# Performance work log

Hardware: AMD Instinct MI355X
Metric: run time of the kernel (lower is better)

## Reference

```python
import jax, jax.numpy as jnp
import numpy as np

B, T = 1024, 1024
D_IN, UNITS, WIDTH, DEPTH, D_OUT = 6, 64, 128, 3, 6
START = UNITS + D_IN  # concat([x_normed, h]) width
EPS = 1e-8


def _xavier(key, fin, fout):
    lim = float(np.sqrt(6.0 / (fin + fout)))
    return jax.random.uniform(key, (fin, fout), minval=-lim, maxval=lim, dtype=jnp.float32)


def setup_inputs() -> dict:
    key = jax.random.key(0)
    ks = jax.random.split(key, 12)
    d = {
        "x": jax.random.normal(ks[0], (B, T, D_IN), dtype=jnp.float32),
        "init_F": jax.random.normal(ks[1], (B, 2 + UNITS), dtype=jnp.float32) * 0.1,
    }
    dims = [START] + [WIDTH] * DEPTH
    for i in range(DEPTH):
        d[f"qb1_w{i}"] = _xavier(ks[2 + 2 * i], dims[i], dims[i + 1])
        d[f"qb1_b{i}"] = jnp.zeros((dims[i + 1],), dtype=jnp.float32)
        d[f"qb2_w{i}"] = _xavier(ks[3 + 2 * i], dims[i], dims[i + 1])
        d[f"qb2_b{i}"] = jnp.zeros((dims[i + 1],), dtype=jnp.float32)
    d["wa"] = _xavier(ks[8], WIDTH, UNITS)
    d["ba"] = jnp.zeros((UNITS,), dtype=jnp.float32)
    d["wb"] = _xavier(ks[9], WIDTH, UNITS)
    d["bb"] = jnp.zeros((UNITS,), dtype=jnp.float32)
    # fc_out bias is frozen at zero in the original -> weight only
    d["wout"] = _xavier(ks[10], UNITS, D_OUT)
    return d


def reference(x, init_F,
              qb1_w0, qb1_b0, qb2_w0, qb2_b0,
              qb1_w1, qb1_b1, qb2_w1, qb2_b1,
              qb1_w2, qb1_b2, qb2_w2, qb2_b2,
              wa, ba, wb, bb, wout):
    layers = ((qb1_w0, qb1_b0, qb2_w0, qb2_b0),
              (qb1_w1, qb1_b1, qb2_w1, qb2_b1),
              (qb1_w2, qb1_b2, qb2_w2, qb2_b2))
    h0 = init_F[:, 2:2 + UNITS]  # [B, UNITS]

    def step(h, xt):  # xt: [B, D_IN], h: [B, UNITS]
        norm = jnp.sqrt(jnp.sum(xt * xt, axis=1, keepdims=True))  # [B,1]
        xn = xt / (norm + EPS)
        c = jnp.concatenate([xn, h], axis=1)  # [B, START]
        for i, (w1, b1, w2, b2) in enumerate(layers):
            x1 = c @ w1 + b1
            x2 = c @ w2 + b2
            if i < DEPTH - 1:
                x1 = jnp.tanh(x1)
                x2 = jnp.tanh(x2)
            c = x1 * x2
        g = jnp.tanh(c)
        alpha = jnp.exp(g @ wa + ba)          # [B, UNITS]
        beta = jnp.tanh(g @ wb + bb)          # [B, UNITS]
        h_new = jnp.exp(-alpha * norm) * (h - beta) + beta
        return h_new, (h_new @ wout, alpha)

    _, (outs, alphas) = jax.lax.scan(step, h0, jnp.swapaxes(x, 0, 1))
    # outs: [T,B,D_OUT], alphas: [T,B,UNITS] -> batch-major
    return jnp.swapaxes(outs, 0, 1), jnp.swapaxes(alphas, 0, 1)
```

## Files before the change

kernel.cpp:

```cpp
#include <hip/hip_runtime.h>
#include <stdint.h>
#include <stddef.h>

#define NB 1024
#define TB 1024
#define D_IN 6
#define UNITS 64
#define WIDTH 128
#define DOUT 6
#define EPSF 1e-8f
#define SPB 16
#define LDK0 108
#define LDK 140

typedef _Float16 v8h __attribute__((ext_vector_type(8)));
typedef float v4f __attribute__((ext_vector_type(4)));

#define MFMAH(A,Bf,C) __builtin_amdgcn_mfma_f32_16x16x32_f16((A),(Bf),(C),0,0,0)

#define BARRIER_LDS() asm volatile("s_waitcnt lgkmcnt(0)\n\ts_barrier" ::: "memory")

#define C2L2E  2.8853900817779268f
#define L2E    1.4426950408889634f
#define NEGL2E (-1.4426950408889634f)

__device__ __forceinline__ float rcp_fast(float x){ return __builtin_amdgcn_rcpf(x); }

__device__ __forceinline__ float tanh_from_arg(float a2){
  float u = __builtin_amdgcn_exp2f(a2);
  return fmaf(-2.0f, rcp_fast(u + 1.0f), 1.0f);
}

__device__ __forceinline__ void make_frag1(const float* vals, v8h& hv){
  #pragma unroll
  for (int j = 0; j < 8; j++) hv[j] = (_Float16)vals[j];
}
__device__ __forceinline__ void make_frag2(const float* vals, v8h& hv, v8h& lv){
  #pragma unroll
  for (int j = 0; j < 8; j++){
    _Float16 h = (_Float16)vals[j];
    hv[j] = h;
    lv[j] = (_Float16)(vals[j] - (float)h);
  }
}

__global__ __launch_bounds__(512, 2) void lmsc_kernel(
    const float* __restrict__ x, const float* __restrict__ initF,
    const float* __restrict__ w10, const float* __restrict__ b10,
    const float* __restrict__ w20, const float* __restrict__ b20,
    const float* __restrict__ w11, const float* __restrict__ b11,
    const float* __restrict__ w21, const float* __restrict__ b21,
    const float* __restrict__ w12, const float* __restrict__ b12,
    const float* __restrict__ w22, const float* __restrict__ b22,
    const float* __restrict__ wa, const float* __restrict__ ba,
    const float* __restrict__ wb, const float* __restrict__ bb,
    const float* __restrict__ wo,
    float* __restrict__ outs, float* __restrict__ alph)
{
  __shared__ __attribute__((aligned(16))) _Float16 c0[2][SPB*LDK0];
  __shared__ __attribute__((aligned(16))) _Float16 cP[SPB*LDK];
  __shared__ __attribute__((aligned(16))) _Float16 cQ[SPB*LDK];
  __shared__ __attribute__((aligned(16))) _Float16 cG[SPB*LDK];
  __shared__ __attribute__((aligned(16))) float nrm[2][SPB];

  const int tid = threadIdx.x;
  const int wv = tid >> 6;
  const int ln = tid & 63;
  const int mn = ln & 15;
  const int qd = ln >> 4;
  const int q8 = qd * 8;
  const int n  = wv * 16 + mn;
  const int sgbase = (int)blockIdx.x * SPB;

  float tmp[8];


  v8h B0[3][2];
  #pragma unroll
  for (int kf = 0; kf < 3; kf++)
    #pragma unroll
    for (int br = 0; br < 2; br++){
      const float* W = br ? w20 : w10;
      #pragma unroll
      for (int j = 0; j < 8; j++){
        int k = kf*32 + q8 + j;
        int r = (k < 6) ? k : ((k >= 8 && k < 72) ? (k - 2) : -1);
        tmp[j] = (r >= 0) ? W[r*WIDTH + n] * C2L2E : 0.0f;
      }
      make_frag1(tmp, B0[kf][br]);
    }

  v8h B1[4][2], B2[4][2];
  #pragma unroll
  for (int kf = 0; kf < 4; kf++)
    #pragma unroll
    for (int br = 0; br < 2; br++){
      const float* W = br ? w21 : w11;
      #pragma unroll
      for (int j = 0; j < 8; j++)
        tmp[j] = W[(kf*32 + q8 + j)*WIDTH + n] * C2L2E;
      make_frag1(tmp, B1[kf][br]);
      const float* V = br ? w22 : w12;
      const float sc = br ? 1.0f : C2L2E;
      #pragma unroll
      for (int j = 0; j < 8; j++)
        tmp[j] = V[(kf*32 + q8 + j)*WIDTH + n] * sc;
      make_frag1(tmp, B2[kf][br]);
    }

  const int u = (wv & 3) * 16 + mn;
  v8h Bah[4], Bal[4], Bbh[4];
  #pragma unroll
  for (int kf = 0; kf < 4; kf++){
    #pragma unroll
    for (int j = 0; j < 8; j++)
      tmp[j] = wa[(kf*32 + q8 + j)*UNITS + u] * L2E;
    make_frag2(tmp, Bah[kf], Bal[kf]);
    #pragma unroll
    for (int j = 0; j < 8; j++)
      tmp[j] = wb[(kf*32 + q8 + j)*UNITS + u] * C2L2E;
    make_frag1(tmp, Bbh[kf]);
  }
  const float bsa = ba[u] * L2E;
  const float bsb = bb[u] * C2L2E;

  v8h Woh0, Woh1;
  #pragma unroll
  for (int j = 0; j < 8; j++)
    tmp[j] = (mn < DOUT) ? wo[(q8 + j)*DOUT + mn] : 0.0f;
  make_frag1(tmp, Woh0);
  #pragma unroll
  for (int j = 0; j < 8; j++)
    tmp[j] = (mn < DOUT) ? wo[(32 + q8 + j)*DOUT + mn] : 0.0f;
  make_frag1(tmp, Woh1);

  const float e0a = b10[n] * C2L2E, e0b = b20[n] * C2L2E;
  const float e1a = b11[n] * C2L2E, e1b = b21[n] * C2L2E;
  const float e2a = b12[n] * C2L2E, e2b = b22[n];

  float* alp  = alph + ((size_t)(sgbase + qd*4) * TB) * UNITS + u;
  float* outp = outs + ((size_t)(sgbase + qd*4) * TB) * DOUT + mn;

  for (int i = tid; i < 2*SPB*LDK0; i += 512) c0[0][i] = (_Float16)0.0f;
  __syncthreads();

  float hreg[4];
  if (wv < 4){
    #pragma unroll
    for (int r = 0; r < 4; r++){
      int s = qd*4 + r;
      float v = initF[(size_t)(sgbase + s)*(2 + UNITS) + 2 + u];
      hreg[r] = v;
      c0[0][s*LDK0 + 8 + u] = (_Float16)v;
    }
  }
  float xv0=0, xv1=0, xv2=0, xv3=0, xv4=0, xv5=0;
  if (wv == 4 && ln < 16){
    const float* xp = x + (size_t)(sgbase + ln)*TB*D_IN;
    float a0=xp[0], a1=xp[1], a2=xp[2], a3=xp[3], a4=xp[4], a5=xp[5];
    float nv = sqrtf(a0*a0 + a1*a1 + a2*a2 + a3*a3 + a4*a4 + a5*a5);
    nrm[0][ln] = nv * NEGL2E;
    float inv = 1.0f / (nv + EPSF);
    c0[0][ln*LDK0 + 0] = (_Float16)(a0*inv);
    c0[0][ln*LDK0 + 1] = (_Float16)(a1*inv);
    c0[0][ln*LDK0 + 2] = (_Float16)(a2*inv);
    c0[0][ln*LDK0 + 3] = (_Float16)(a3*inv);
    c0[0][ln*LDK0 + 4] = (_Float16)(a4*inv);
    c0[0][ln*LDK0 + 5] = (_Float16)(a5*inv);
    xv0 = xp[6]; xv1 = xp[7]; xv2 = xp[8]; xv3 = xp[9]; xv4 = xp[10]; xv5 = xp[11];
  }
  __syncthreads();

  auto wout_phase = [&](const _Float16* cb, int tt){
    v8h ah0 = *(const v8h*)(cb + mn*LDK0 + 8 + q8);
    v8h ah1 = *(const v8h*)(cb + mn*LDK0 + 40 + q8);
    v4f acc = {0.f, 0.f, 0.f, 0.f};
    acc = MFMAH(ah0, Woh0, acc);
    acc = MFMAH(ah1, Woh1, acc);
    if (mn < DOUT){
      #pragma unroll
      for (int r = 0; r < 4; r++)
        outp[(size_t)r*TB*DOUT + (size_t)tt*DOUT] = acc[r];
    }
  };

  for (int t = 0; t < TB; t++){
    const int p = t & 1;
    const _Float16* c0r = c0[p];
    _Float16* c0w = c0[p ^ 1];

    {
      v8h ah[3];
      #pragma unroll
      for (int kf = 0; kf < 3; kf++)
        ah[kf] = *(const v8h*)(c0r + mn*LDK0 + kf*32 + q8);
      v4f acc0 = {e0a, e0a, e0a, e0a};
      v4f acc1 = {e0b, e0b, e0b, e0b};
      #pragma unroll
      for (int kf = 0; kf < 3; kf++){
        acc0 = MFMAH(ah[kf], B0[kf][0], acc0);
        acc1 = MFMAH(ah[kf], B0[kf][1], acc1);
      }
      #pragma unroll
      for (int r = 0; r < 4; r++){
        float u0 = __builtin_amdgcn_exp2f(acc0[r]);
        float u1 = __builtin_amdgcn_exp2f(acc1[r]);
        float pr = u0 * u1;
        float sm = u0 + u1;
        float pp = pr + 1.0f;
        float res = (pp - sm) * rcp_fast(pp + sm);
        cP[(qd*4 + r)*LDK + n] = (_Float16)res;
      }
    }
    BARRIER_LDS();

    {
      v8h ah[4];
      #pragma unroll
      for (int kf = 0; kf < 4; kf++)
        ah[kf] = *(const v8h*)(cP + mn*LDK + kf*32 + q8);
      v4f acc0 = {e1a, e1a, e1a, e1a};
      v4f acc1 = {e1b, e1b, e1b, e1b};
      #pragma unroll
      for (int kf = 0; kf < 4; kf++){
        acc0 = MFMAH(ah[kf], B1[kf][0], acc0);
        acc1 = MFMAH(ah[kf], B1[kf][1], acc1);
      }
      #pragma unroll
      for (int r = 0; r < 4; r++){
        float u0 = __builtin_amdgcn_exp2f(acc0[r]);
        float u1 = __builtin_amdgcn_exp2f(acc1[r]);
        float pr = u0 * u1;
        float sm = u0 + u1;
        float pp = pr + 1.0f;
        float res = (pp - sm) * rcp_fast(pp + sm);
        cQ[(qd*4 + r)*LDK + n] = (_Float16)res;
      }
    }
    BARRIER_LDS();

    {
      v8h ah[4];
      #pragma unroll
      for (int kf = 0; kf < 4; kf++)
        ah[kf] = *(const v8h*)(cQ + mn*LDK + kf*32 + q8);
      v4f acc0 = {e2a, e2a, e2a, e2a};
      v4f acc1 = {e2b, e2b, e2b, e2b};
      #pragma unroll
      for (int kf = 0; kf < 4; kf++){
        acc0 = MFMAH(ah[kf], B2[kf][0], acc0);
        acc1 = MFMAH(ah[kf], B2[kf][1], acc1);
      }
      #pragma unroll
      for (int r = 0; r < 4; r++)
        cG[(qd*4 + r)*LDK + n] = (_Float16)tanh_from_arg(acc0[r] * acc1[r]);
    }
    BARRIER_LDS();

    if (wv < 4){
      v8h gh[4];
      #pragma unroll
      for (int kf = 0; kf < 4; kf++)
        gh[kf] = *(const v8h*)(cG + mn*LDK + kf*32 + q8);
      v4f pA0 = {bsa, bsa, bsa, bsa};
      v4f pA1 = {0.f, 0.f, 0.f, 0.f};
      v4f pB  = {bsb, bsb, bsb, bsb};
      #pragma unroll
      for (int kf = 0; kf < 2; kf++){
        pA0 = MFMAH(gh[kf], Bah[kf], pA0);
        pA0 = MFMAH(gh[kf], Bal[kf], pA0);
        pA1 = MFMAH(gh[kf+2], Bah[kf+2], pA1);
        pA1 = MFMAH(gh[kf+2], Bal[kf+2], pA1);
        pB  = MFMAH(gh[2*kf],   Bbh[2*kf],   pB);
        pB  = MFMAH(gh[2*kf+1], Bbh[2*kf+1], pB);
      }
      #pragma unroll
      for (int r = 0; r < 4; r++){
        int s = qd*4 + r;
        float m = nrm[p][s];
        float alpha = __builtin_amdgcn_exp2f(pA0[r] + pA1[r]);
        float beta  = tanh_from_arg(pB[r]);
        float dec   = __builtin_amdgcn_exp2f(alpha * m);
        float h = fmaf(dec, hreg[r] - beta, beta);
        hreg[r] = h;
        c0w[s*LDK0 + 8 + u] = (_Float16)h;
        alp[(size_t)r*TB*UNITS] = alpha;
      }
      alp += UNITS;
    } else if (wv == 7){
      if (t > 0) wout_phase(c0r, t - 1);
    } else if (wv == 4 && ln < 16){
      float nv2 = sqrtf(xv0*xv0 + xv1*xv1 + xv2*xv2 + xv3*xv3 + xv4*xv4 + xv5*xv5);
      nrm[p ^ 1][ln] = nv2 * NEGL2E;
      float inv = 1.0f / (nv2 + EPSF);
      c0w[ln*LDK0 + 0] = (_Float16)(xv0*inv);
      c0w[ln*LDK0 + 1] = (_Float16)(xv1*inv);
      c0w[ln*LDK0 + 2] = (_Float16)(xv2*inv);
      c0w[ln*LDK0 + 3] = (_Float16)(xv3*inv);
      c0w[ln*LDK0 + 4] = (_Float16)(xv4*inv);
      c0w[ln*LDK0 + 5] = (_Float16)(xv5*inv);
      int tn = t + 2; if (tn > TB - 1) tn = TB - 1;
      const float* xp = x + ((size_t)(sgbase + ln)*TB + (size_t)tn)*D_IN;
      xv0 = xp[0]; xv1 = xp[1]; xv2 = xp[2]; xv3 = xp[3]; xv4 = xp[4]; xv5 = xp[5];
    }
    BARRIER_LDS();
  }

  if (wv == 7) wout_phase(c0[TB & 1], TB - 1);
}

extern "C" void kernel_launch(void* const* d_in, const int* in_sizes, int n_in,
                              void* d_out, int out_size, void* d_ws, size_t ws_size,
                              hipStream_t stream) {
  const float* x    = (const float*)d_in[0];
  const float* iF   = (const float*)d_in[1];
  const float* w10  = (const float*)d_in[2];
  const float* b10  = (const float*)d_in[3];
  const float* w20  = (const float*)d_in[4];
  const float* b20  = (const float*)d_in[5];
  const float* w11  = (const float*)d_in[6];
  const float* b11  = (const float*)d_in[7];
  const float* w21  = (const float*)d_in[8];
  const float* b21  = (const float*)d_in[9];
  const float* w12  = (const float*)d_in[10];
  const float* b12  = (const float*)d_in[11];
  const float* w22  = (const float*)d_in[12];
  const float* b22  = (const float*)d_in[13];
  const float* wa   = (const float*)d_in[14];
  const float* ba   = (const float*)d_in[15];
  const float* wb   = (const float*)d_in[16];
  const float* bb   = (const float*)d_in[17];
  const float* wo   = (const float*)d_in[18];

  float* outs = (float*)d_out;
  float* alph = outs + (size_t)NB*TB*DOUT;

  lmsc_kernel<<<NB/SPB, 512, 0, stream>>>(x, iF,
      w10, b10, w20, b20, w11, b11, w21, b21, w12, b12, w22, b22,
      wa, ba, wb, bb, wo, outs, alph);
}
```

Before: 2.291 ms.

## Shrink blocks to two sequences each for more blocks, move head weights to LDS

Each block now handles 2 batch sequences instead of 16, using 4 waves of 256 threads. Each wave computes two 16-column groups of the hidden layers, so the grid grows from 64 to 512 blocks and fills many more CUs for this latency-bound recurrence. The MFMA tiles stay 16 rows tall, so 14 of every 16 rows are padding and compute is wasted. To ease register pressure, some alpha/beta/output weight fragments move to LDS and are reloaded every step, which adds LDS traffic.

New measurement: 5.328 ms. 133% more time.

```diff
diff --git a/kernel.cpp b/kernel.cpp
--- a/kernel.cpp
+++ b/kernel.cpp
@@ -9,12 +9,14 @@
 #define WIDTH 128
 #define DOUT 6
 #define EPSF 1e-8f
-#define SPB 16
+#define SPB 2
+#define ROWS 16
 #define LDK0 108
 #define LDK 140
 
 typedef _Float16 v8h __attribute__((ext_vector_type(8)));
 typedef float v4f __attribute__((ext_vector_type(4)));
+typedef float v2f __attribute__((ext_vector_type(2)));
 
 #define MFMAH(A,Bf,C) __builtin_amdgcn_mfma_f32_16x16x32_f16((A),(Bf),(C),0,0,0)
 
@@ -44,7 +46,7 @@
   }
 }
 
-__global__ __launch_bounds__(512, 2) void lmsc_kernel(
+__global__ __launch_bounds__(256, 2) void lmsc_kernel(
     const float* __restrict__ x, const float* __restrict__ initF,
     const float* __restrict__ w10, const float* __restrict__ b10,
     const float* __restrict__ w20, const float* __restrict__ b20,
@@ -57,11 +59,13 @@
     const float* __restrict__ wo,
     float* __restrict__ outs, float* __restrict__ alph)
 {
-  __shared__ __attribute__((aligned(16))) _Float16 c0[2][SPB*LDK0];
-  __shared__ __attribute__((aligned(16))) _Float16 cP[SPB*LDK];
-  __shared__ __attribute__((aligned(16))) _Float16 cQ[SPB*LDK];
-  __shared__ __attribute__((aligned(16))) _Float16 cG[SPB*LDK];
-  __shared__ __attribute__((aligned(16))) float nrm[2][SPB];
+  __shared__ __attribute__((aligned(16))) _Float16 c0[2][ROWS*LDK0];
+  __shared__ __attribute__((aligned(16))) _Float16 cP[ROWS*LDK];
+  __shared__ __attribute__((aligned(16))) _Float16 cQ[ROWS*LDK];
+  __shared__ __attribute__((aligned(16))) _Float16 cG[ROWS*LDK];
+  __shared__ __attribute__((aligned(16))) _Float16 fragD[8][256][8];
+  __shared__ __attribute__((aligned(16))) _Float16 fragW[2][256][8];
+  __shared__ __attribute__((aligned(16))) float nrm[2][ROWS];
 
   const int tid = threadIdx.x;
   const int wv = tid >> 6;
@@ -69,117 +73,136 @@
   const int mn = ln & 15;
   const int qd = ln >> 4;
   const int q8 = qd * 8;
-  const int n  = wv * 16 + mn;
+  const int n0 = wv * 16 + mn;
+  const int n1 = n0 + 64;
+  const int u  = wv * 16 + mn;
   const int sgbase = (int)blockIdx.x * SPB;
 
   float tmp[8];
 
-
-  v8h B0[3][2];
-  #pragma unroll
-  for (int kf = 0; kf < 3; kf++)
-    #pragma unroll
-    for (int br = 0; br < 2; br++){
-      const float* W = br ? w20 : w10;
-      #pragma unroll
-      for (int j = 0; j < 8; j++){
-        int k = kf*32 + q8 + j;
-        int r = (k < 6) ? k : ((k >= 8 && k < 72) ? (k - 2) : -1);
-        tmp[j] = (r >= 0) ? W[r*WIDTH + n] * C2L2E : 0.0f;
-      }
-      make_frag1(tmp, B0[kf][br]);
-    }
-
-  v8h B1[4][2], B2[4][2];
-  #pragma unroll
-  for (int kf = 0; kf < 4; kf++)
-    #pragma unroll
-    for (int br = 0; br < 2; br++){
-      const float* W = br ? w21 : w11;
-      #pragma unroll
-      for (int j = 0; j < 8; j++)
-        tmp[j] = W[(kf*32 + q8 + j)*WIDTH + n] * C2L2E;
-      make_frag1(tmp, B1[kf][br]);
-      const float* V = br ? w22 : w12;
-      const float sc = br ? 1.0f : C2L2E;
-      #pragma unroll
-      for (int j = 0; j < 8; j++)
-        tmp[j] = V[(kf*32 + q8 + j)*WIDTH + n] * sc;
-      make_frag1(tmp, B2[kf][br]);
-    }
-
-  const int u = (wv & 3) * 16 + mn;
-  v8h Bah[4], Bal[4], Bbh[4];
+  v8h B0[2][3][2];
+  #pragma unroll
+  for (int g = 0; g < 2; g++)
+    #pragma unroll
+    for (int kf = 0; kf < 3; kf++)
+      #pragma unroll
+      for (int br = 0; br < 2; br++){
+        const float* W = br ? w20 : w10;
+        const int nc = g ? n1 : n0;
+        #pragma unroll
+        for (int j = 0; j < 8; j++){
+          int k = kf*32 + q8 + j;
+          int r = (k < 6) ? k : ((k >= 8 && k < 72) ? (k - 2) : -1);
+          tmp[j] = (r >= 0) ? W[r*WIDTH + nc] * C2L2E : 0.0f;
+        }
+        make_frag1(tmp, B0[g][kf][br]);
+      }
+
+  v8h B1[2][4][2], B2[2][4][2];
+  #pragma unroll
+  for (int g = 0; g < 2; g++)
+    #pragma unroll
+    for (int kf = 0; kf < 4; kf++)
+      #pragma unroll
+      for (int br = 0; br < 2; br++){
+        const int nc = g ? n1 : n0;
+        const float* W = br ? w21 : w11;
+        #pragma unroll
+        for (int j = 0; j < 8; j++)
+          tmp[j] = W[(kf*32 + q8 + j)*WIDTH + nc] * C2L2E;
+        make_frag1(tmp, B1[g][kf][br]);
+        const float* V = br ? w22 : w12;
+        const float sc = br ? 1.0f : C2L2E;
+        #pragma unroll
+        for (int j = 0; j < 8; j++)
+          tmp[j] = V[(kf*32 + q8 + j)*WIDTH + nc] * sc;
+        make_frag1(tmp, B2[g][kf][br]);
+      }
+
+  v8h Bah[4];
   #pragma unroll
   for (int kf = 0; kf < 4; kf++){
     #pragma unroll
     for (int j = 0; j < 8; j++)
       tmp[j] = wa[(kf*32 + q8 + j)*UNITS + u] * L2E;
-    make_frag2(tmp, Bah[kf], Bal[kf]);
+    v8h lv;
+    make_frag2(tmp, Bah[kf], lv);
+    *(v8h*)&fragD[kf][tid][0] = lv;
     #pragma unroll
     for (int j = 0; j < 8; j++)
       tmp[j] = wb[(kf*32 + q8 + j)*UNITS + u] * C2L2E;
-    make_frag1(tmp, Bbh[kf]);
+    v8h bv;
+    make_frag1(tmp, bv);
+    *(v8h*)&fragD[4 + kf][tid][0] = bv;
   }
   const float bsa = ba[u] * L2E;
   const float bsb = bb[u] * C2L2E;
 
-  v8h Woh0, Woh1;
-  #pragma unroll
-  for (int j = 0; j < 8; j++)
-    tmp[j] = (mn < DOUT) ? wo[(q8 + j)*DOUT + mn] : 0.0f;
-  make_frag1(tmp, Woh0);
-  #pragma unroll
-  for (int j = 0; j < 8; j++)
-    tmp[j] = (mn < DOUT) ? wo[(32 + q8 + j)*DOUT + mn] : 0.0f;
-  make_frag1(tmp, Woh1);
-
-  const float e0a = b10[n] * C2L2E, e0b = b20[n] * C2L2E;
-  const float e1a = b11[n] * C2L2E, e1b = b21[n] * C2L2E;
-  const float e2a = b12[n] * C2L2E, e2b = b22[n];
-
-  float* alp  = alph + ((size_t)(sgbase + qd*4) * TB) * UNITS + u;
-  float* outp = outs + ((size_t)(sgbase + qd*4) * TB) * DOUT + mn;
-
-  for (int i = tid; i < 2*SPB*LDK0; i += 512) c0[0][i] = (_Float16)0.0f;
+  {
+    #pragma unroll
+    for (int j = 0; j < 8; j++)
+      tmp[j] = (mn < DOUT) ? wo[(q8 + j)*DOUT + mn] : 0.0f;
+    v8h w0h; make_frag1(tmp, w0h);
+    *(v8h*)&fragW[0][tid][0] = w0h;
+    #pragma unroll
+    for (int j = 0; j < 8; j++)
+      tmp[j] = (mn < DOUT) ? wo[(32 + q8 + j)*DOUT + mn] : 0.0f;
+    v8h w1h; make_frag1(tmp, w1h);
+    *(v8h*)&fragW[1][tid][0] = w1h;
+  }
+
+  const float e0a[2] = {b10[n0]*C2L2E, b10[n1]*C2L2E};
+  const float e0b[2] = {b20[n0]*C2L2E, b20[n1]*C2L2E};
+  const float e1a[2] = {b11[n0]*C2L2E, b11[n1]*C2L2E};
+  const float e1b[2] = {b21[n0]*C2L2E, b21[n1]*C2L2E};
+  const float e2a[2] = {b12[n0]*C2L2E, b12[n1]*C2L2E};
+  const float e2b[2] = {b22[n0],       b22[n1]};
+
+  float* alp  = alph + ((size_t)sgbase * TB) * UNITS + u;
+  float* outp = outs + ((size_t)sgbase * TB) * DOUT + mn;
+
+  for (int i = tid; i < 2*ROWS*LDK0; i += 256) c0[0][i] = (_Float16)0.0f;
+  if (tid < ROWS){ nrm[0][tid] = 0.0f; nrm[1][tid] = 0.0f; }
   __syncthreads();
 
-  float hreg[4];
-  if (wv < 4){
-    #pragma unroll
-    for (int r = 0; r < 4; r++){
-      int s = qd*4 + r;
-      float v = initF[(size_t)(sgbase + s)*(2 + UNITS) + 2 + u];
+  float hreg[SPB] = {0.0f, 0.0f};
+  if (qd == 0){
+    #pragma unroll
+    for (int r = 0; r < SPB; r++){
+      float v = initF[(size_t)(sgbase + r)*(2 + UNITS) + 2 + u];
       hreg[r] = v;
-      c0[0][s*LDK0 + 8 + u] = (_Float16)v;
+      c0[0][r*LDK0 + 8 + u] = (_Float16)v;
     }
   }
   float xv0=0, xv1=0, xv2=0, xv3=0, xv4=0, xv5=0;
-  if (wv == 4 && ln < 16){
-    const float* xp = x + (size_t)(sgbase + ln)*TB*D_IN;
-    float a0=xp[0], a1=xp[1], a2=xp[2], a3=xp[3], a4=xp[4], a5=xp[5];
-    float nv = sqrtf(a0*a0 + a1*a1 + a2*a2 + a3*a3 + a4*a4 + a5*a5);
+  if (wv == 1 && ln < SPB){
+    const v2f* xp2 = (const v2f*)(x + (size_t)(sgbase + ln)*TB*D_IN);
+    v2f A = xp2[0], Bv = xp2[1], C = xp2[2];
+    float nv = sqrtf(A[0]*A[0] + A[1]*A[1] + Bv[0]*Bv[0] + Bv[1]*Bv[1] + C[0]*C[0] + C[1]*C[1]);
     nrm[0][ln] = nv * NEGL2E;
     float inv = 1.0f / (nv + EPSF);
-    c0[0][ln*LDK0 + 0] = (_Float16)(a0*inv);
-    c0[0][ln*LDK0 + 1] = (_Float16)(a1*inv);
-    c0[0][ln*LDK0 + 2] = (_Float16)(a2*inv);
-    c0[0][ln*LDK0 + 3] = (_Float16)(a3*inv);
-    c0[0][ln*LDK0 + 4] = (_Float16)(a4*inv);
-    c0[0][ln*LDK0 + 5] = (_Float16)(a5*inv);
-    xv0 = xp[6]; xv1 = xp[7]; xv2 = xp[8]; xv3 = xp[9]; xv4 = xp[10]; xv5 = xp[11];
+    c0[0][ln*LDK0 + 0] = (_Float16)(A[0]*inv);
+    c0[0][ln*LDK0 + 1] = (_Float16)(A[1]*inv);
+    c0[0][ln*LDK0 + 2] = (_Float16)(Bv[0]*inv);
+    c0[0][ln*LDK0 + 3] = (_Float16)(Bv[1]*inv);
+    c0[0][ln*LDK0 + 4] = (_Float16)(C[0]*inv);
+    c0[0][ln*LDK0 + 5] = (_Float16)(C[1]*inv);
+    v2f D = xp2[3], E = xp2[4], F = xp2[5];
+    xv0 = D[0]; xv1 = D[1]; xv2 = E[0]; xv3 = E[1]; xv4 = F[0]; xv5 = F[1];
   }
   __syncthreads();
 
   auto wout_phase = [&](const _Float16* cb, int tt){
     v8h ah0 = *(const v8h*)(cb + mn*LDK0 + 8 + q8);
     v8h ah1 = *(const v8h*)(cb + mn*LDK0 + 40 + q8);
+    v8h W0 = *(const v8h*)&fragW[0][tid][0];
+    v8h W1 = *(const v8h*)&fragW[1][tid][0];
     v4f acc = {0.f, 0.f, 0.f, 0.f};
-    acc = MFMAH(ah0, Woh0, acc);
-    acc = MFMAH(ah1, Woh1, acc);
-    if (mn < DOUT){
-      #pragma unroll
-      for (int r = 0; r < 4; r++)
+    acc = MFMAH(ah0, W0, acc);
+    acc = MFMAH(ah1, W1, acc);
+    if (mn < DOUT && qd == 0){
+      #pragma unroll
+      for (int r = 0; r < SPB; r++)
         outp[(size_t)r*TB*DOUT + (size_t)tt*DOUT] = acc[r];
     }
   };
@@ -194,23 +217,29 @@
       #pragma unroll
       for (int kf = 0; kf < 3; kf++)
         ah[kf] = *(const v8h*)(c0r + mn*LDK0 + kf*32 + q8);
-      v4f acc0 = {e0a, e0a, e0a, e0a};
-      v4f acc1 = {e0b, e0b, e0b, e0b};
-      #pragma unroll
-      for (int kf = 0; kf < 3; kf++){
-        acc0 = MFMAH(ah[kf], B0[kf][0], acc0);
-        acc1 = MFMAH(ah[kf], B0[kf][1], acc1);
-      }
-      #pragma unroll
-      for (int r = 0; r < 4; r++){
-        float u0 = __builtin_amdgcn_exp2f(acc0[r]);
-        float u1 = __builtin_amdgcn_exp2f(acc1[r]);
-        float pr = u0 * u1;
-        float sm = u0 + u1;
-        float pp = pr + 1.0f;
-        float res = (pp - sm) * rcp_fast(pp + sm);
-        cP[(qd*4 + r)*LDK + n] = (_Float16)res;
-      }
+      v4f a0[2], a1[2];
+      #pragma unroll
+      for (int g = 0; g < 2; g++){
+        a0[g] = (v4f){e0a[g], e0a[g], e0a[g], e0a[g]};
+        a1[g] = (v4f){e0b[g], e0b[g], e0b[g], e0b[g]};
+      }
+      #pragma unroll
+      for (int kf = 0; kf < 3; kf++)
+        #pragma unroll
+        for (int g = 0; g < 2; g++){
+          a0[g] = MFMAH(ah[kf], B0[g][kf][0], a0[g]);
+          a1[g] = MFMAH(ah[kf], B0[g][kf][1], a1[g]);
+        }
+      #pragma unroll
+      for (int g = 0; g < 2; g++)
+        #pragma unroll
+        for (int r = 0; r < SPB; r++){
+          float u0 = __builtin_amdgcn_exp2f(a0[g][r]);
+          float u1 = __builtin_amdgcn_exp2f(a1[g][r]);
+          float pp = fmaf(u0, u1, 1.0f);
+          float sm = u0 + u1;
+          cP[(qd*4 + r)*LDK + (g ? n1 : n0)] = (_Float16)((pp - sm) * rcp_fast(pp + sm));
+        }
     }
     BARRIER_LDS();
 
@@ -219,23 +248,29 @@
       #pragma unroll
       for (int kf = 0; kf < 4; kf++)
         ah[kf] = *(const v8h*)(cP + mn*LDK + kf*32 + q8);
-      v4f acc0 = {e1a, e1a, e1a, e1a};
-      v4f acc1 = {e1b, e1b, e1b, e1b};
-      #pragma unroll
-      for (int kf = 0; kf < 4; kf++){
-        acc0 = MFMAH(ah[kf], B1[kf][0], acc0);
-        acc1 = MFMAH(ah[kf], B1[kf][1], acc1);
-      }
-      #pragma unroll
-      for (int r = 0; r < 4; r++){
-        float u0 = __builtin_amdgcn_exp2f(acc0[r]);
-        float u1 = __builtin_amdgcn_exp2f(acc1[r]);
-        float pr = u0 * u1;
-        float sm = u0 + u1;
-        float pp = pr + 1.0f;
-        float res = (pp - sm) * rcp_fast(pp + sm);
-        cQ[(qd*4 + r)*LDK + n] = (_Float16)res;
-      }
+      v4f a0[2], a1[2];
+      #pragma unroll
+      for (int g = 0; g < 2; g++){
+        a0[g] = (v4f){e1a[g], e1a[g], e1a[g], e1a[g]};
+        a1[g] = (v4f){e1b[g], e1b[g], e1b[g], e1b[g]};
+      }
+      #pragma unroll
+      for (int kf = 0; kf < 4; kf++)
+        #pragma unroll
+        for (int g = 0; g < 2; g++){
+          a0[g] = MFMAH(ah[kf], B1[g][kf][0], a0[g]);
+          a1[g] = MFMAH(ah[kf], B1[g][kf][1], a1[g]);
+        }
+      #pragma unroll
+      for (int g = 0; g < 2; g++)
+        #pragma unroll
+        for (int r = 0; r < SPB; r++){
+          float u0 = __builtin_amdgcn_exp2f(a0[g][r]);
+          float u1 = __builtin_amdgcn_exp2f(a1[g][r]);
+          float pp = fmaf(u0, u1, 1.0f);
+          float sm = u0 + u1;
+          cQ[(qd*4 + r)*LDK + (g ? n1 : n0)] = (_Float16)((pp - sm) * rcp_fast(pp + sm));
+        }
     }
     BARRIER_LDS();
 
@@ -244,52 +279,64 @@
       #pragma unroll
       for (int kf = 0; kf < 4; kf++)
         ah[kf] = *(const v8h*)(cQ + mn*LDK + kf*32 + q8);
-      v4f acc0 = {e2a, e2a, e2a, e2a};
-      v4f acc1 = {e2b, e2b, e2b, e2b};
+      v4f a0[2], a1[2];
+      #pragma unroll
+      for (int g = 0; g < 2; g++){
+        a0[g] = (v4f){e2a[g], e2a[g], e2a[g], e2a[g]};
+        a1[g] = (v4f){e2b[g], e2b[g], e2b[g], e2b[g]};
+      }
+      #pragma unroll
+      for (int kf = 0; kf < 4; kf++)
+        #pragma unroll
+        for (int g = 0; g < 2; g++){
+          a0[g] = MFMAH(ah[kf], B2[g][kf][0], a0[g]);
+          a1[g] = MFMAH(ah[kf], B2[g][kf][1], a1[g]);
+        }
+      #pragma unroll
+      for (int g = 0; g < 2; g++)
+        #pragma unroll
+        for (int r = 0; r < SPB; r++)
+          cG[(qd*4 + r)*LDK + (g ? n1 : n0)] = (_Float16)tanh_from_arg(a0[g][r] * a1[g][r]);
+    }
+    BARRIER_LDS();
+
+    {
+      v8h gh[4];
+      #pragma unroll
+      for (int kf = 0; kf < 4; kf++)
+        gh[kf] = *(const v8h*)(cG + mn*LDK + kf*32 + q8);
+      v8h BalL[4], BbhL[4];
       #pragma unroll
       for (int kf = 0; kf < 4; kf++){
-        acc0 = MFMAH(ah[kf], B2[kf][0], acc0);
-        acc1 = MFMAH(ah[kf], B2[kf][1], acc1);
-      }
-      #pragma unroll
-      for (int r = 0; r < 4; r++)
-        cG[(qd*4 + r)*LDK + n] = (_Float16)tanh_from_arg(acc0[r] * acc1[r]);
-    }
-    BARRIER_LDS();
-
-    if (wv < 4){
-      v8h gh[4];
-      #pragma unroll
-      for (int kf = 0; kf < 4; kf++)
-        gh[kf] = *(const v8h*)(cG + mn*LDK + kf*32 + q8);
+        BalL[kf] = *(const v8h*)&fragD[kf][tid][0];
+        BbhL[kf] = *(const v8h*)&fragD[4 + kf][tid][0];
+      }
       v4f pA0 = {bsa, bsa, bsa, bsa};
       v4f pA1 = {0.f, 0.f, 0.f, 0.f};
       v4f pB  = {bsb, bsb, bsb, bsb};
       #pragma unroll
       for (int kf = 0; kf < 2; kf++){
         pA0 = MFMAH(gh[kf], Bah[kf], pA0);
-        pA0 = MFMAH(gh[kf], Bal[kf], pA0);
+        pA0 = MFMAH(gh[kf], BalL[kf], pA0);
         pA1 = MFMAH(gh[kf+2], Bah[kf+2], pA1);
-        pA1 = MFMAH(gh[kf+2], Bal[kf+2], pA1);
-        pB  = MFMAH(gh[2*kf],   Bbh[2*kf],   pB);
-        pB  = MFMAH(gh[2*kf+1], Bbh[2*kf+1], pB);
-      }
-      #pragma unroll
-      for (int r = 0; r < 4; r++){
-        int s = qd*4 + r;
-        float m = nrm[p][s];
+        pA1 = MFMAH(gh[kf+2], BalL[kf+2], pA1);
+        pB  = MFMAH(gh[2*kf],   BbhL[2*kf],   pB);
+        pB  = MFMAH(gh[2*kf+1], BbhL[2*kf+1], pB);
+      }
+      #pragma unroll
+      for (int r = 0; r < SPB; r++){
+        float m = nrm[p][qd*4 + r];
         float alpha = __builtin_amdgcn_exp2f(pA0[r] + pA1[r]);
         float beta  = tanh_from_arg(pB[r]);
         float dec   = __builtin_amdgcn_exp2f(alpha * m);
         float h = fmaf(dec, hreg[r] - beta, beta);
         hreg[r] = h;
-        c0w[s*LDK0 + 8 + u] = (_Float16)h;
-        alp[(size_t)r*TB*UNITS] = alpha;
+        c0w[(qd*4 + r)*LDK0 + 8 + u] = (_Float16)h;
+        if (qd == 0) alp[(size_t)r*TB*UNITS] = alpha;
       }
       alp += UNITS;
-    } else if (wv == 7){
-      if (t > 0) wout_phase(c0r, t - 1);
-    } else if (wv == 4 && ln < 16){
+    }
+    if (wv == 1 && ln < SPB){
       float nv2 = sqrtf(xv0*xv0 + xv1*xv1 + xv2*xv2 + xv3*xv3 + xv4*xv4 + xv5*xv5);
       nrm[p ^ 1][ln] = nv2 * NEGL2E;
       float inv = 1.0f / (nv2 + EPSF);
@@ -300,13 +347,16 @@
       c0w[ln*LDK0 + 4] = (_Float16)(xv4*inv);
       c0w[ln*LDK0 + 5] = (_Float16)(xv5*inv);
       int tn = t + 2; if (tn > TB - 1) tn = TB - 1;
-      const float* xp = x + ((size_t)(sgbase + ln)*TB + (size_t)tn)*D_IN;
-      xv0 = xp[0]; xv1 = xp[1]; xv2 = xp[2]; xv3 = xp[3]; xv4 = xp[4]; xv5 = xp[5];
+      const v2f* xp2 = (const v2f*)(x + ((size_t)(sgbase + ln)*TB + (size_t)tn)*D_IN);
+      v2f D = xp2[0], E = xp2[1], F = xp2[2];
+      xv0 = D[0]; xv1 = D[1]; xv2 = E[0]; xv3 = E[1]; xv4 = F[0]; xv5 = F[1];
+    } else if (wv == 2){
+      if (t > 0) wout_phase(c0r, t - 1);
     }
     BARRIER_LDS();
   }
 
-  if (wv == 7) wout_phase(c0[TB & 1], TB - 1);
+  if (wv == 2) wout_phase(c0[0], TB - 1);
 }
 
 extern "C" void kernel_launch(void* const* d_in, const int* in_sizes, int n_in,
@@ -335,7 +385,7 @@
   float* outs = (float*)d_out;
   float* alph = outs + (size_t)NB*TB*DOUT;
 
-  lmsc_kernel<<<NB/SPB, 512, 0, stream>>>(x, iF,
+  lmsc_kernel<<<NB/SPB, 256, 0, stream>>>(x, iF,
       w10, b10, w20, b20, w11, b11, w21, b21, w12, b12, w22, b22,
       wa, ba, wb, bb, wo, outs, alph);
 }
```
